# Kernel tuning notes

Hardware: AMD Instinct MI355X
Metric: run time of the kernel (lower is better)

## Reference

```python
import jax, jax.numpy as jnp
import numpy as np

B, T, C, V = 4, 2048, 512, 32000


def setup_inputs() -> dict:
    key = jax.random.key(0)
    ks = jax.random.split(key, 8)
    return {
        "idx": jax.random.randint(ks[0], (B, T), 0, V, dtype=jnp.int64 if jax.config.jax_enable_x64 else jnp.int32),
        "targets": jax.random.randint(ks[1], (B, T), 0, V, dtype=jnp.int64 if jax.config.jax_enable_x64 else jnp.int32),
        "token_emb": jax.random.normal(ks[2], (V, C), jnp.float32) * 0.02,
        "pos_emb": jax.random.normal(ks[3], (T, C), jnp.float32) * 0.02,
        "Wk": jax.random.normal(ks[4], (C, C), jnp.float32) / np.sqrt(C),
        "Wq": jax.random.normal(ks[5], (C, C), jnp.float32) / np.sqrt(C),
        "Wv": jax.random.normal(ks[6], (C, C), jnp.float32) / np.sqrt(C),
        "Wo": jax.random.normal(ks[7], (C, V), jnp.float32) / np.sqrt(C),
        "bo": jnp.zeros((V,), jnp.float32),
    }


def reference(idx, targets, token_emb, pos_emb, Wk, Wq, Wv, Wo, bo):
    # embeddings: token lookup + positional add  -> [B, T, C]
    x = token_emb[idx] + pos_emb[None, :idx.shape[1]]
    # single self-attention head (scale uses input dim C, per source)
    q = x @ Wq  # [B, T, C]
    k = x @ Wk
    v = x @ Wv
    wei = jnp.einsum("btc,bsc->bts", q, k) * (C ** -0.5)  # [B, T, T]
    mask = jnp.tril(jnp.ones((idx.shape[1], idx.shape[1]), bool))
    wei = jnp.where(mask[None], wei, -jnp.inf)
    wei = jax.nn.softmax(wei, axis=-1)
    attn = jnp.einsum("bts,bsc->btc", wei, v)  # [B, T, C]
    logits = attn @ Wo + bo  # [B, T, V]
    # cross-entropy (mean over B*T), matching F.cross_entropy
    logp = jax.nn.log_softmax(logits, axis=-1)
    nll = -jnp.take_along_axis(logp, targets[..., None], axis=-1)[..., 0]
    loss = nll.mean()
    return logits, loss
```

## Files before the change

kernel.cpp:

```cpp
#include <hip/hip_runtime.h>
#include <cstdint>

typedef unsigned short u16;
typedef __attribute__((ext_vector_type(8))) short short8;
typedef __attribute__((ext_vector_type(4))) float f32x4;

constexpr int kB = 4, kT = 2048, kC = 512, kV = 32000;
constexpr int kBT = kB * kT;
constexpr float kScale = 0.044194173824159216f;

__device__ __forceinline__ u16 f2b(float f) {
  union { float f; unsigned u; } v; v.f = f;
  unsigned r = v.u + 0x7fffu + ((v.u >> 16) & 1u);
  return (u16)(r >> 16);
}

__device__ __forceinline__ void g2lds16(const u16* g, u16* l) {
  __builtin_amdgcn_global_load_lds(
      (const __attribute__((address_space(1))) void*)g,
      (__attribute__((address_space(3))) void*)l, 16, 0, 0);
}

__global__ __launch_bounds__(256) void transpose_cast(const float* __restrict__ in,
                                                      u16* __restrict__ out,
                                                      int R, int Ncol) {
  __shared__ u16 tile[32][33];
  int c0 = blockIdx.x * 32, r0 = blockIdx.y * 32;
  int tx = threadIdx.x, ty = threadIdx.y;
#pragma unroll
  for (int j = 0; j < 32; j += 8)
    tile[ty + j][tx] = f2b(in[(long)(r0 + ty + j) * Ncol + (c0 + tx)]);
  __syncthreads();
#pragma unroll
  for (int j = 0; j < 32; j += 8)
    out[(long)(c0 + ty + j) * R + (r0 + tx)] = tile[tx][ty + j];
}

__global__ __launch_bounds__(128) void embed_kernel(const int* __restrict__ idx,
                                                    const float* __restrict__ te,
                                                    const float* __restrict__ pe,
                                                    u16* __restrict__ xb) {
  int row = blockIdx.x;
  int t = row & (kT - 1);
  int tok = idx[row];
  int c = threadIdx.x * 4;
  float4 a = *(const float4*)(te + (long)tok * kC + c);
  float4 p = *(const float4*)(pe + (long)t * kC + c);
  ushort4 o;
  o.x = f2b(a.x + p.x); o.y = f2b(a.y + p.y);
  o.z = f2b(a.z + p.z); o.w = f2b(a.w + p.w);
  *(ushort4*)(xb + (long)row * kC + c) = o;
}

template <int OUT_MODE, bool CAUSAL, bool KCAP>
__global__ __launch_bounds__(256) void gemm_bt(
    const u16* __restrict__ A, const u16* __restrict__ Bt, void* __restrict__ OutP,
    const float* __restrict__ bias,
    int M, int N, int K, int lda, int ldb, int ldo,
    long batchA, long batchB, long batchO, float alpha) {
  int bz = blockIdx.z;
  A += bz * batchA;
  Bt += bz * batchB;
  int m0 = blockIdx.y * 128, n0 = blockIdx.x * 128;
  if (CAUSAL && n0 > m0 + 127) return;

  __shared__ u16 As[2][128 * 32];
  __shared__ u16 Bs[2][128 * 32];
  int tid = threadIdx.x;
  int lane = tid & 63, w = tid >> 6;
  int wr = w >> 1, wc = w & 1;
  int lm = lane & 15, lk = lane >> 4;

  f32x4 acc[4][4] = {};

  const u16* aptr = A + (long)(m0 + (w << 4) + (lane >> 2)) * lda + ((lane & 3) << 3);
  const u16* bptr = Bt + (long)(n0 + (w << 4) + (lane >> 2)) * ldb + ((lane & 3) << 3);

#define STAGE(buf)                                                   \
  {                                                                  \
    g2lds16(aptr,                  &As[buf][(w << 4) * 32]);         \
    g2lds16(aptr + (long)64 * lda, &As[buf][(64 + (w << 4)) * 32]);  \
    g2lds16(bptr,                  &Bs[buf][(w << 4) * 32]);         \
    g2lds16(bptr + (long)64 * ldb, &Bs[buf][(64 + (w << 4)) * 32]);  \
  }

  int nk = K >> 5;
  if (KCAP) { int cap = (m0 >> 5) + 4; nk = (cap < nk) ? cap : nk; }
  STAGE(0);
  __syncthreads();

  for (int kt = 0; kt < nk; ++kt) {
    int cur = kt & 1;
    aptr += 32; bptr += 32;
    if (kt + 1 < nk) STAGE(cur ^ 1);
    short8 af[4], bf[4];
#pragma unroll
    for (int i = 0; i < 4; ++i) {
      af[i] = *(const short8*)&As[cur][(wr * 64 + i * 16 + lm) * 32 + lk * 8];
      bf[i] = *(const short8*)&Bs[cur][(wc * 64 + i * 16 + lm) * 32 + lk * 8];
    }
#pragma unroll
    for (int mi = 0; mi < 4; ++mi)
#pragma unroll
      for (int ni = 0; ni < 4; ++ni)
        acc[mi][ni] = __builtin_amdgcn_mfma_f32_16x16x32_bf16(af[mi], bf[ni], acc[mi][ni], 0, 0, 0);
    __syncthreads();
  }
#undef STAGE

#pragma unroll
  for (int mi = 0; mi < 4; ++mi) {
#pragma unroll
    for (int ni = 0; ni < 4; ++ni) {
      int row = m0 + wr * 64 + mi * 16 + lk * 4;
      int col = n0 + wc * 64 + ni * 16 + lm;
      if (OUT_MODE == 0) {
        float* Out = (float*)OutP + bz * batchO;
        float bv = bias ? bias[col] : 0.0f;
#pragma unroll
        for (int r = 0; r < 4; ++r)
          Out[(long)(row + r) * ldo + col] = acc[mi][ni][r] * alpha + bv;
      } else if (OUT_MODE == 1) {
        u16* Out = (u16*)OutP + bz * batchO;
#pragma unroll
        for (int r = 0; r < 4; ++r)
          Out[(long)(row + r) * ldo + col] = f2b(acc[mi][ni][r] * alpha);
      } else {
        u16* Out = (u16*)OutP + bz * batchO;
        ushort4 pk;
        pk.x = f2b(acc[mi][ni][0] * alpha);
        pk.y = f2b(acc[mi][ni][1] * alpha);
        pk.z = f2b(acc[mi][ni][2] * alpha);
        pk.w = f2b(acc[mi][ni][3] * alpha);
        *(ushort4*)&Out[(long)col * ldo + row] = pk;
      }
    }
  }
}

__global__ __launch_bounds__(512, 2) void gemm256_logits_ce(
    const u16* __restrict__ A, const u16* __restrict__ Bt,
    float* __restrict__ Out, const float* __restrict__ bias,
    float* __restrict__ cepart) {
  constexpr int lda = kC, ldb = kC, ldo = kV;
  constexpr int nk = kC / 64;
  constexpr int NB = kV / 256;

  __shared__ u16 lds[65536];

  int wg = blockIdx.x;
  int xcd = wg & 7;
  int i = wg >> 3;
  int g = i >> 5, r = i & 31;
  int bx = (g < 15) ? (g * 8 + (r >> 2)) : (120 + (r >> 2));
  int by = xcd * 4 + (r & 3);
  int m0 = by * 256, n0 = bx * 256;

  int tid = threadIdx.x;
  int lane = tid & 63, w = tid >> 6;
  int wm = w >> 2, wn = w & 3;
  int lm = lane & 15, lk = lane >> 4;
  int lk16 = lk * 16, sw = (lm & 7) << 4;
  int brow0 = (wn & 1) * 64;

  int srow = tid >> 3;
  int scol = ((tid & 7) ^ ((tid >> 3) & 7)) * 8;
  const u16* Arow = A + (long)(m0 + srow) * lda + scol;
  const u16* Brow = Bt + (long)(n0 + srow) * ldb + scol;

  f32x4 acc[8][4] = {};
  short8 aF[4][2], bF[4][2];

  auto stage = [&](int s) {
    if (s >= 4 * nk) return;
    int tile = s >> 2, hf = s & 3, buf = tile & 1;
    int kofs = tile * 64;
    if (hf >= 2) {
      u16* base = &lds[(buf * 2 + (hf - 2)) * 8192 + w * 512];
      const u16* gp = Arow + (long)((hf - 2) * 128) * lda + kofs;
      g2lds16(gp, base);
      g2lds16(gp + (long)64 * lda, base + 4096);
    } else {
      u16* base = &lds[32768 + (buf * 2 + hf) * 8192 + w * 512];
      const u16* gp = Brow + (long)(hf * 128) * ldb + kofs;
      g2lds16(gp, base);
      g2lds16(gp + (long)64 * ldb, base + 4096);
    }
  };

#pragma unroll
  for (int s = 0; s < 6; ++s) stage(s);
  asm volatile("s_waitcnt vmcnt(4)" ::: "memory");
  __builtin_amdgcn_sched_barrier(0);
  __builtin_amdgcn_s_barrier();

#pragma unroll 2
  for (int t = 0; t < nk; ++t) {
    int cur = t & 1;
    const char* Ab = (const char*)&lds[(cur * 2 + wm) * 8192];
    const char* Bb = (const char*)&lds[32768 + (cur * 2 + (wn >> 1)) * 8192];

#define RDA(i, ks) (*(const short8*)(Ab + (((qr)*4 + (i)) * 16 + lm) * 128 + (((ks)*64 + lk16) ^ sw)))
#define RDB(j, ks) (*(const short8*)(Bb + (brow0 + ((qc)*2 + (j)) * 16 + lm) * 128 + (((ks)*64 + lk16) ^ sw)))
#define MFMA_QUAD                                                              \
  _Pragma("unroll") for (int i = 0; i < 4; ++i)                                \
  _Pragma("unroll") for (int j = 0; j < 2; ++j)                                \
  _Pragma("unroll") for (int ks = 0; ks < 2; ++ks)                             \
      acc[qr * 4 + i][qc * 2 + j] = __builtin_amdgcn_mfma_f32_16x16x32_bf16(   \
          aF[i][ks], bF[qc * 2 + j][ks], acc[qr * 4 + i][qc * 2 + j], 0, 0, 0);

    {
      constexpr int qr = 0, qc = 0;
#pragma unroll
      for (int i = 0; i < 4; ++i) { aF[i][0] = RDA(i, 0); aF[i][1] = RDA(i, 1); }
#pragma unroll
      for (int j = 0; j < 2; ++j) { bF[j][0] = RDB(j, 0); bF[j][1] = RDB(j, 1); }
      stage(4 * (t + 1) + 2);
      stage(4 * (t + 1) + 3);
      __builtin_amdgcn_s_barrier();
      asm volatile("s_waitcnt lgkmcnt(0)" ::: "memory");
      __builtin_amdgcn_s_setprio(1);
      MFMA_QUAD
      __builtin_amdgcn_s_setprio(0);
      __builtin_amdgcn_s_barrier();
    }
    {
      constexpr int qr = 0, qc = 1;
#pragma unroll
      for (int j = 0; j < 2; ++j) { bF[2 + j][0] = RDB(j, 0); bF[2 + j][1] = RDB(j, 1); }
      __builtin_amdgcn_s_barrier();
      asm volatile("s_waitcnt lgkmcnt(0)" ::: "memory");
      __builtin_amdgcn_s_setprio(1);
      MFMA_QUAD
      __builtin_amdgcn_s_setprio(0);
      __builtin_amdgcn_s_barrier();
    }
    {
      constexpr int qr = 1, qc = 0;
#pragma unroll
      for (int i = 0; i < 4; ++i) { aF[i][0] = RDA(i, 0); aF[i][1] = RDA(i, 1); }
      __builtin_amdgcn_s_barrier();
      asm volatile("s_waitcnt lgkmcnt(0)" ::: "memory");
      __builtin_amdgcn_s_setprio(1);
      MFMA_QUAD
      __builtin_amdgcn_s_setprio(0);
      __builtin_amdgcn_s_barrier();
    }
    {
      constexpr int qr = 1, qc = 1;
      stage(4 * (t + 2) + 0);
      stage(4 * (t + 2) + 1);
      __builtin_amdgcn_s_barrier();
      asm volatile("s_waitcnt lgkmcnt(0)" ::: "memory");
      __builtin_amdgcn_s_setprio(1);
      MFMA_QUAD
      __builtin_amdgcn_s_setprio(0);
      if (t < nk - 2) {
        asm volatile("s_waitcnt vmcnt(4)" ::: "memory");
        __builtin_amdgcn_sched_barrier(0);
      } else if (t == nk - 2) {
        asm volatile("s_waitcnt vmcnt(0)" ::: "memory");
        __builtin_amdgcn_sched_barrier(0);
      }
      __builtin_amdgcn_s_barrier();
    }
#undef RDA
#undef RDB
#undef MFMA_QUAD
  }

  float* lds_ce = (float*)lds;
#pragma unroll
  for (int rf = 0; rf < 8; ++rf) {
    int grow = m0 + wm * 128 + rf * 16 + lk * 4;
    float rowsum[4] = {};
#pragma unroll
    for (int cf = 0; cf < 4; ++cf) {
      int col = n0 + wn * 64 + cf * 16 + lm;
      float bv = bias[col];
#pragma unroll
      for (int r = 0; r < 4; ++r) {
        float v = acc[rf][cf][r] + bv;
        __builtin_nontemporal_store(v, &Out[(long)(grow + r) * ldo + col]);
        rowsum[r] += __expf(v);
      }
    }
#pragma unroll
    for (int off = 1; off < 16; off <<= 1)
#pragma unroll
      for (int r = 0; r < 4; ++r)
        rowsum[r] += __shfl_xor(rowsum[r], off, 64);
    if (lm == 0) {
#pragma unroll
      for (int r = 0; r < 4; ++r)
        lds_ce[w * 128 + rf * 16 + lk * 4 + r] = rowsum[r];
    }
  }
  __syncthreads();
  if (tid < 256) {
    int wmg = tid >> 7, r128 = tid & 127;
    float s = lds_ce[(wmg * 4 + 0) * 128 + r128] + lds_ce[(wmg * 4 + 1) * 128 + r128]
            + lds_ce[(wmg * 4 + 2) * 128 + r128] + lds_ce[(wmg * 4 + 3) * 128 + r128];
    cepart[(long)(m0 + tid) * NB + bx] = s;
  }
}

__global__ __launch_bounds__(256) void softmax_causal(const float* __restrict__ S,
                                                      u16* __restrict__ P) {
  int row = blockIdx.x;
  int t = row & (kT - 1);
  int lim = ((t >> 7) + 1) << 7;
  const float* srow = S + (long)row * kT;
  u16* prow = P + (long)row * kT;
  __shared__ float buf[kT];
  __shared__ float red[256];
  int tid = threadIdx.x;
  float mx = -1e30f;
  for (int s = tid; s < lim; s += 256) {
    float v = (s <= t) ? srow[s] : -1e30f;
    buf[s] = v;
    mx = fmaxf(mx, v);
  }
  red[tid] = mx; __syncthreads();
  for (int o = 128; o > 0; o >>= 1) {
    if (tid < o) red[tid] = fmaxf(red[tid], red[tid + o]);
    __syncthreads();
  }
  mx = red[0]; __syncthreads();
  float sm = 0.0f;
  for (int s = tid; s < lim; s += 256) {
    float e = (s <= t) ? __expf(buf[s] - mx) : 0.0f;
    buf[s] = e;
    sm += e;
  }
  red[tid] = sm; __syncthreads();
  for (int o = 128; o > 0; o >>= 1) {
    if (tid < o) red[tid] += red[tid + o];
    __syncthreads();
  }
  float inv = 1.0f / red[0];
  for (int s = tid; s < lim; s += 256) prow[s] = f2b(buf[s] * inv);
}

__global__ __launch_bounds__(256) void ce_reduce(const float* __restrict__ logits,
                                                 const float* __restrict__ part,
                                                 const int* __restrict__ targets,
                                                 float* __restrict__ nll, int P) {
  int row = blockIdx.x * 4 + (threadIdx.x >> 6);
  int lane = threadIdx.x & 63;
  const float* pr = part + (long)row * P;
  float s = 0.0f;
  for (int p = lane; p < P; p += 64) s += pr[p];
#pragma unroll
  for (int off = 1; off < 64; off <<= 1) s += __shfl_xor(s, off, 64);
  if (lane == 0)
    nll[row] = __logf(s) - logits[(long)row * kV + targets[row]];
}

__global__ __launch_bounds__(256) void loss_reduce(const float* __restrict__ nll,
                                                   float* __restrict__ out) {
  __shared__ float red[256];
  int tid = threadIdx.x;
  float s = 0.0f;
  for (int i = tid; i < kBT; i += 256) s += nll[i];
  red[tid] = s; __syncthreads();
  for (int o = 128; o > 0; o >>= 1) {
    if (tid < o) red[tid] += red[tid + o];
    __syncthreads();
  }
  if (tid == 0) out[0] = red[0] / (float)kBT;
}

extern "C" void kernel_launch(void* const* d_in, const int* in_sizes, int n_in,
                              void* d_out, int out_size, void* d_ws, size_t ws_size,
                              hipStream_t stream) {
  const int* idx       = (const int*)d_in[0];
  const int* targets   = (const int*)d_in[1];
  const float* token_e = (const float*)d_in[2];
  const float* pos_e   = (const float*)d_in[3];
  const float* Wk      = (const float*)d_in[4];
  const float* Wq      = (const float*)d_in[5];
  const float* Wv      = (const float*)d_in[6];
  const float* Wo      = (const float*)d_in[7];
  const float* bo      = (const float*)d_in[8];
  float* out = (float*)d_out;

  char* ws = (char*)d_ws;
  size_t need = 0;
  auto alloc = [&](size_t bytes) { char* p = ws + need; need += (bytes + 255) & ~(size_t)255; return p; };
  u16* xb   = (u16*)alloc((size_t)kBT * kC * 2);
  u16* wqt  = (u16*)alloc((size_t)kC * kC * 2);
  u16* wkt  = (u16*)alloc((size_t)kC * kC * 2);
  u16* wvt  = (u16*)alloc((size_t)kC * kC * 2);
  u16* wot  = (u16*)alloc((size_t)kV * kC * 2);
  u16* qb   = (u16*)alloc((size_t)kBT * kC * 2);
  u16* kb   = (u16*)alloc((size_t)kBT * kC * 2);
  u16* vt   = (u16*)alloc((size_t)kC * kBT * 2);
  u16* attn = (u16*)alloc((size_t)kBT * kC * 2);
  float* nll = (float*)alloc((size_t)kBT * 4);
  if (ws_size < need) return;

  float* cepart = (float*)qb;

  float* Sbuf = out;
  u16* Pbuf   = (u16*)((char*)d_out + (100ull << 20));

  dim3 tb(32, 8);
  transpose_cast<<<dim3(kC / 32, kC / 32), tb, 0, stream>>>(Wq, wqt, kC, kC);
  transpose_cast<<<dim3(kC / 32, kC / 32), tb, 0, stream>>>(Wk, wkt, kC, kC);
  transpose_cast<<<dim3(kC / 32, kC / 32), tb, 0, stream>>>(Wv, wvt, kC, kC);
  transpose_cast<<<dim3(kV / 32, kC / 32), tb, 0, stream>>>(Wo, wot, kC, kV);

  embed_kernel<<<kBT, 128, 0, stream>>>(idx, token_e, pos_e, xb);

  gemm_bt<1, false, false><<<dim3(4, 64, 2), 256, 0, stream>>>(xb, wqt, qb, nullptr,
      kBT, kC, kC, kC, kC, kC, 0, (long)kC * kC, (long)kBT * kC, 1.0f);
  gemm_bt<2, false, false><<<dim3(4, 64, 1), 256, 0, stream>>>(xb, wvt, vt, nullptr,
      kBT, kC, kC, kC, kC, kBT, 0, 0, 0, 1.0f);

  gemm_bt<0, true, false><<<dim3(16, 16, 4), 256, 0, stream>>>(qb, kb, Sbuf, nullptr,
      kT, kT, kC, kC, kC, kT, (long)kT * kC, (long)kT * kC, (long)kT * kT, kScale);

  softmax_causal<<<kBT, 256, 0, stream>>>(Sbuf, Pbuf);

  gemm_bt<1, false, true><<<dim3(4, 16, 4), 256, 0, stream>>>(Pbuf, vt, attn, nullptr,
      kT, kC, kT, kT, kBT, kC, (long)kT * kT, (long)kT, (long)kT * kC, 1.0f);

  gemm256_logits_ce<<<dim3((kV / 256) * (kBT / 256)), 512, 0, stream>>>(
      attn, wot, out, bo, cepart);

  ce_reduce<<<kBT / 4, 256, 0, stream>>>(out, cepart, targets, nll, kV / 256);
  loss_reduce<<<1, 256, 0, stream>>>(nll, out + (long)kBT * kV);
}
```

Measured before the change: 563.5 us.

## Process two M tiles per workgroup and prefetch second tile during epilogue

The logits GEMM+CE kernel now gives each workgroup two consecutive 256-row M tiles for one N column, halving the grid to 2000 blocks. The second tile's global-to-LDS prologue loads are issued before the first tile's logits stores and row-sum reduction, so the epilogue overlaps with the next tile's memory traffic. The CE partial scratch moves to an LDS region the prologue does not touch. The B tile is still reloaded for the second pass, and the longer per-block runtime changes wave scheduling across CUs.

```diff
diff --git a/kernel.cpp b/kernel.cpp
--- a/kernel.cpp
+++ b/kernel.cpp
@@ -150,11 +150,10 @@
 
   int wg = blockIdx.x;
   int xcd = wg & 7;
-  int i = wg >> 3;
-  int g = i >> 5, r = i & 31;
-  int bx = (g < 15) ? (g * 8 + (r >> 2)) : (120 + (r >> 2));
-  int by = xcd * 4 + (r & 3);
-  int m0 = by * 256, n0 = bx * 256;
+  int j = wg >> 3;
+  int by0 = xcd * 4 + (j & 1) * 2;
+  int bx = j >> 1;
+  int n0 = bx * 256;
 
   int tid = threadIdx.x;
   int lane = tid & 63, w = tid >> 6;
@@ -165,19 +164,28 @@
 
   int srow = tid >> 3;
   int scol = ((tid & 7) ^ ((tid >> 3) & 7)) * 8;
-  const u16* Arow = A + (long)(m0 + srow) * lda + scol;
-  const u16* Brow = Bt + (long)(n0 + srow) * ldb + scol;
-
-  f32x4 acc[8][4] = {};
+  const u16* Arow0 = A + (long)(by0 * 256 + srow) * lda + scol;
+  const u16* Arow1 = Arow0 + (long)256 * lda;
+  const u16* Brow  = Bt + (long)(n0 + srow) * ldb + scol;
+
+  f32x4 acc[8][4];
   short8 aF[4][2], bF[4][2];
 
-  auto stage = [&](int s) {
+  auto zeroAcc = [&]() {
+#pragma unroll
+    for (int rf = 0; rf < 8; ++rf)
+#pragma unroll
+      for (int cf = 0; cf < 4; ++cf)
+        acc[rf][cf] = (f32x4){0.f, 0.f, 0.f, 0.f};
+  };
+
+  auto stage = [&](const u16* Ar, int s) {
     if (s >= 4 * nk) return;
     int tile = s >> 2, hf = s & 3, buf = tile & 1;
     int kofs = tile * 64;
     if (hf >= 2) {
       u16* base = &lds[(buf * 2 + (hf - 2)) * 8192 + w * 512];
-      const u16* gp = Arow + (long)((hf - 2) * 128) * lda + kofs;
+      const u16* gp = Ar + (long)((hf - 2) * 128) * lda + kofs;
       g2lds16(gp, base);
       g2lds16(gp + (long)64 * lda, base + 4096);
     } else {
@@ -188,121 +196,150 @@
     }
   };
 
-#pragma unroll
-  for (int s = 0; s < 6; ++s) stage(s);
+  auto kloop = [&](const u16* Ar) {
+#pragma unroll 2
+    for (int t = 0; t < nk; ++t) {
+      int cur = t & 1;
+      const char* Ab = (const char*)&lds[(cur * 2 + wm) * 8192];
+      const char* Bb = (const char*)&lds[32768 + (cur * 2 + (wn >> 1)) * 8192];
+
+#define RDA(i, ks) (*(const short8*)(Ab + (((qr)*4 + (i)) * 16 + lm) * 128 + (((ks)*64 + lk16) ^ sw)))
+#define RDB(jj, ks) (*(const short8*)(Bb + (brow0 + ((qc)*2 + (jj)) * 16 + lm) * 128 + (((ks)*64 + lk16) ^ sw)))
+#define MFMA_QUAD                                                              \
+  _Pragma("unroll") for (int i = 0; i < 4; ++i)                                \
+  _Pragma("unroll") for (int jj = 0; jj < 2; ++jj)                             \
+  _Pragma("unroll") for (int ks = 0; ks < 2; ++ks)                             \
+      acc[qr * 4 + i][qc * 2 + jj] = __builtin_amdgcn_mfma_f32_16x16x32_bf16(  \
+          aF[i][ks], bF[qc * 2 + jj][ks], acc[qr * 4 + i][qc * 2 + jj], 0, 0, 0);
+
+      {
+        constexpr int qr = 0, qc = 0;
+#pragma unroll
+        for (int i = 0; i < 4; ++i) { aF[i][0] = RDA(i, 0); aF[i][1] = RDA(i, 1); }
+#pragma unroll
+        for (int jj = 0; jj < 2; ++jj) { bF[jj][0] = RDB(jj, 0); bF[jj][1] = RDB(jj, 1); }
+        stage(Ar, 4 * (t + 1) + 2);
+        stage(Ar, 4 * (t + 1) + 3);
+        __builtin_amdgcn_s_barrier();
+        asm volatile("s_waitcnt lgkmcnt(0)" ::: "memory");
+        __builtin_amdgcn_s_setprio(1);
+        MFMA_QUAD
+        __builtin_amdgcn_s_setprio(0);
+        __builtin_amdgcn_s_barrier();
+      }
+      {
+        constexpr int qr = 0, qc = 1;
+#pragma unroll
+        for (int jj = 0; jj < 2; ++jj) { bF[2 + jj][0] = RDB(jj, 0); bF[2 + jj][1] = RDB(jj, 1); }
+        __builtin_amdgcn_s_barrier();
+        asm volatile("s_waitcnt lgkmcnt(0)" ::: "memory");
+        __builtin_amdgcn_s_setprio(1);
+        MFMA_QUAD
+        __builtin_amdgcn_s_setprio(0);
+        __builtin_amdgcn_s_barrier();
+      }
+      {
+        constexpr int qr = 1, qc = 0;
+#pragma unroll
+        for (int i = 0; i < 4; ++i) { aF[i][0] = RDA(i, 0); aF[i][1] = RDA(i, 1); }
+        __builtin_amdgcn_s_barrier();
+        asm volatile("s_waitcnt lgkmcnt(0)" ::: "memory");
+        __builtin_amdgcn_s_setprio(1);
+        MFMA_QUAD
+        __builtin_amdgcn_s_setprio(0);
+        __builtin_amdgcn_s_barrier();
+      }
+      {
+        constexpr int qr = 1, qc = 1;
+        stage(Ar, 4 * (t + 2) + 0);
+        stage(Ar, 4 * (t + 2) + 1);
+        __builtin_amdgcn_s_barrier();
+        asm volatile("s_waitcnt lgkmcnt(0)" ::: "memory");
+        __builtin_amdgcn_s_setprio(1);
+        MFMA_QUAD
+        __builtin_amdgcn_s_setprio(0);
+        if (t < nk - 2) {
+          asm volatile("s_waitcnt vmcnt(4)" ::: "memory");
+          __builtin_amdgcn_sched_barrier(0);
+        } else if (t == nk - 2) {
+          asm volatile("s_waitcnt vmcnt(0)" ::: "memory");
+          __builtin_amdgcn_sched_barrier(0);
+        }
+        __builtin_amdgcn_s_barrier();
+      }
+#undef RDA
+#undef RDB
+#undef MFMA_QUAD
+    }
+  };
+
+  auto storeTile = [&](int m0) {
+#pragma unroll
+    for (int rf = 0; rf < 8; ++rf) {
+      int grow = m0 + wm * 128 + rf * 16 + lk * 4;
+#pragma unroll
+      for (int cf = 0; cf < 4; ++cf) {
+        int col = n0 + wn * 64 + cf * 16 + lm;
+        float bv = bias[col];
+#pragma unroll
+        for (int r = 0; r < 4; ++r)
+          __builtin_nontemporal_store(acc[rf][cf][r] + bv, &Out[(long)(grow + r) * ldo + col]);
+      }
+    }
+  };
+
+  auto ceEmit = [&](int m0) {
+    float* lds_ce = (float*)&lds[16384];
+#pragma unroll
+    for (int rf = 0; rf < 8; ++rf) {
+      float rowsum[4] = {};
+#pragma unroll
+      for (int cf = 0; cf < 4; ++cf) {
+        float bv = bias[n0 + wn * 64 + cf * 16 + lm];
+#pragma unroll
+        for (int r = 0; r < 4; ++r)
+          rowsum[r] += __expf(acc[rf][cf][r] + bv);
+      }
+#pragma unroll
+      for (int off = 1; off < 16; off <<= 1)
+#pragma unroll
+        for (int r = 0; r < 4; ++r)
+          rowsum[r] += __shfl_xor(rowsum[r], off, 64);
+      if (lm == 0) {
+#pragma unroll
+        for (int r = 0; r < 4; ++r)
+          lds_ce[w * 128 + rf * 16 + lk * 4 + r] = rowsum[r];
+      }
+    }
+    __syncthreads();
+    if (tid < 256) {
+      int wmg = tid >> 7, r128 = tid & 127;
+      float s = lds_ce[(wmg * 4 + 0) * 128 + r128] + lds_ce[(wmg * 4 + 1) * 128 + r128]
+              + lds_ce[(wmg * 4 + 2) * 128 + r128] + lds_ce[(wmg * 4 + 3) * 128 + r128];
+      cepart[(long)(m0 + tid) * NB + bx] = s;
+    }
+  };
+
+  zeroAcc();
+#pragma unroll
+  for (int s = 0; s < 6; ++s) stage(Arow0, s);
   asm volatile("s_waitcnt vmcnt(4)" ::: "memory");
   __builtin_amdgcn_sched_barrier(0);
   __builtin_amdgcn_s_barrier();
-
-#pragma unroll 2
-  for (int t = 0; t < nk; ++t) {
-    int cur = t & 1;
-    const char* Ab = (const char*)&lds[(cur * 2 + wm) * 8192];
-    const char* Bb = (const char*)&lds[32768 + (cur * 2 + (wn >> 1)) * 8192];
-
-#define RDA(i, ks) (*(const short8*)(Ab + (((qr)*4 + (i)) * 16 + lm) * 128 + (((ks)*64 + lk16) ^ sw)))
-#define RDB(j, ks) (*(const short8*)(Bb + (brow0 + ((qc)*2 + (j)) * 16 + lm) * 128 + (((ks)*64 + lk16) ^ sw)))
-#define MFMA_QUAD                                                              \
-  _Pragma("unroll") for (int i = 0; i < 4; ++i)                                \
-  _Pragma("unroll") for (int j = 0; j < 2; ++j)                                \
-  _Pragma("unroll") for (int ks = 0; ks < 2; ++ks)                             \
-      acc[qr * 4 + i][qc * 2 + j] = __builtin_amdgcn_mfma_f32_16x16x32_bf16(   \
-          aF[i][ks], bF[qc * 2 + j][ks], acc[qr * 4 + i][qc * 2 + j], 0, 0, 0);
-
-    {
-      constexpr int qr = 0, qc = 0;
-#pragma unroll
-      for (int i = 0; i < 4; ++i) { aF[i][0] = RDA(i, 0); aF[i][1] = RDA(i, 1); }
-#pragma unroll
-      for (int j = 0; j < 2; ++j) { bF[j][0] = RDB(j, 0); bF[j][1] = RDB(j, 1); }
-      stage(4 * (t + 1) + 2);
-      stage(4 * (t + 1) + 3);
-      __builtin_amdgcn_s_barrier();
-      asm volatile("s_waitcnt lgkmcnt(0)" ::: "memory");
-      __builtin_amdgcn_s_setprio(1);
-      MFMA_QUAD
-      __builtin_amdgcn_s_setprio(0);
-      __builtin_amdgcn_s_barrier();
-    }
-    {
-      constexpr int qr = 0, qc = 1;
-#pragma unroll
-      for (int j = 0; j < 2; ++j) { bF[2 + j][0] = RDB(j, 0); bF[2 + j][1] = RDB(j, 1); }
-      __builtin_amdgcn_s_barrier();
-      asm volatile("s_waitcnt lgkmcnt(0)" ::: "memory");
-      __builtin_amdgcn_s_setprio(1);
-      MFMA_QUAD
-      __builtin_amdgcn_s_setprio(0);
-      __builtin_amdgcn_s_barrier();
-    }
-    {
-      constexpr int qr = 1, qc = 0;
-#pragma unroll
-      for (int i = 0; i < 4; ++i) { aF[i][0] = RDA(i, 0); aF[i][1] = RDA(i, 1); }
-      __builtin_amdgcn_s_barrier();
-      asm volatile("s_waitcnt lgkmcnt(0)" ::: "memory");
-      __builtin_amdgcn_s_setprio(1);
-      MFMA_QUAD
-      __builtin_amdgcn_s_setprio(0);
-      __builtin_amdgcn_s_barrier();
-    }
-    {
-      constexpr int qr = 1, qc = 1;
-      stage(4 * (t + 2) + 0);
-      stage(4 * (t + 2) + 1);
-      __builtin_amdgcn_s_barrier();
-      asm volatile("s_waitcnt lgkmcnt(0)" ::: "memory");
-      __builtin_amdgcn_s_setprio(1);
-      MFMA_QUAD
-      __builtin_amdgcn_s_setprio(0);
-      if (t < nk - 2) {
-        asm volatile("s_waitcnt vmcnt(4)" ::: "memory");
-        __builtin_amdgcn_sched_barrier(0);
-      } else if (t == nk - 2) {
-        asm volatile("s_waitcnt vmcnt(0)" ::: "memory");
-        __builtin_amdgcn_sched_barrier(0);
-      }
-      __builtin_amdgcn_s_barrier();
-    }
-#undef RDA
-#undef RDB
-#undef MFMA_QUAD
-  }
-
-  float* lds_ce = (float*)lds;
-#pragma unroll
-  for (int rf = 0; rf < 8; ++rf) {
-    int grow = m0 + wm * 128 + rf * 16 + lk * 4;
-    float rowsum[4] = {};
-#pragma unroll
-    for (int cf = 0; cf < 4; ++cf) {
-      int col = n0 + wn * 64 + cf * 16 + lm;
-      float bv = bias[col];
-#pragma unroll
-      for (int r = 0; r < 4; ++r) {
-        float v = acc[rf][cf][r] + bv;
-        __builtin_nontemporal_store(v, &Out[(long)(grow + r) * ldo + col]);
-        rowsum[r] += __expf(v);
-      }
-    }
-#pragma unroll
-    for (int off = 1; off < 16; off <<= 1)
-#pragma unroll
-      for (int r = 0; r < 4; ++r)
-        rowsum[r] += __shfl_xor(rowsum[r], off, 64);
-    if (lm == 0) {
-#pragma unroll
-      for (int r = 0; r < 4; ++r)
-        lds_ce[w * 128 + rf * 16 + lk * 4 + r] = rowsum[r];
-    }
-  }
-  __syncthreads();
-  if (tid < 256) {
-    int wmg = tid >> 7, r128 = tid & 127;
-    float s = lds_ce[(wmg * 4 + 0) * 128 + r128] + lds_ce[(wmg * 4 + 1) * 128 + r128]
-            + lds_ce[(wmg * 4 + 2) * 128 + r128] + lds_ce[(wmg * 4 + 3) * 128 + r128];
-    cepart[(long)(m0 + tid) * NB + bx] = s;
-  }
+  kloop(Arow0);
+
+#pragma unroll
+  for (int s = 0; s < 6; ++s) stage(Arow1, s);
+  storeTile(by0 * 256);
+  ceEmit(by0 * 256);
+  asm volatile("s_waitcnt vmcnt(0)" ::: "memory");
+  __builtin_amdgcn_sched_barrier(0);
+  __builtin_amdgcn_s_barrier();
+
+  zeroAcc();
+  kloop(Arow1);
+  ceEmit((by0 + 1) * 256);
+  storeTile((by0 + 1) * 256);
 }
 
 __global__ __launch_bounds__(256) void softmax_causal(const float* __restrict__ S,
@@ -426,8 +463,7 @@
   gemm_bt<1, false, true><<<dim3(4, 16, 4), 256, 0, stream>>>(Pbuf, vt, attn, nullptr,
       kT, kC, kT, kT, kBT, kC, (long)kT * kT, (long)kT, (long)kT * kC, 1.0f);
 
-  gemm256_logits_ce<<<dim3((kV / 256) * (kBT / 256)), 512, 0, stream>>>(
-      attn, wot, out, bo, cepart);
+  gemm256_logits_ce<<<dim3(2000), 512, 0, stream>>>(attn, wot, out, bo, cepart);
 
   ce_reduce<<<kBT / 4, 256, 0, stream>>>(out, cepart, targets, nll, kV / 256);
   loss_reduce<<<1, 256, 0, stream>>>(nll, out + (long)kBT * kV);
```

Result: slower. 578.4 us (+2.6%).
